# Performance work log

Hardware: AMD Instinct MI355X
Metric: run time of the kernel (lower is better)

The kernel has to match this reference:

```python
import jax, jax.numpy as jnp
import numpy as np

EMBED_DIM = 512
N_HEADS = 16
HEAD_DIM = EMBED_DIM // N_HEADS  # 32


def setup_inputs() -> dict:
    key0 = jax.random.key(0)
    ks = jax.random.split(key0, 8)
    B, S, D = 4, 2048, EMBED_DIM
    inp = {
        "key": jax.random.normal(ks[0], (B, S, D), dtype=jnp.float32),
        "query": jax.random.normal(ks[1], (B, S, D), dtype=jnp.float32),
        "value": jax.random.normal(ks[2], (B, S, D), dtype=jnp.float32),
        # per-head projection weights (nn.Linear: y = x @ W.T), no bias
        "Wq": jax.random.normal(ks[3], (HEAD_DIM, HEAD_DIM), dtype=jnp.float32) * 0.1,
        "Wk": jax.random.normal(ks[4], (HEAD_DIM, HEAD_DIM), dtype=jnp.float32) * 0.1,
        "Wv": jax.random.normal(ks[5], (HEAD_DIM, HEAD_DIM), dtype=jnp.float32) * 0.1,
        # output projection with bias
        "Wo": jax.random.normal(ks[6], (EMBED_DIM, EMBED_DIM), dtype=jnp.float32) * 0.05,
        "bo": jax.random.normal(ks[7], (EMBED_DIM,), dtype=jnp.float32) * 0.01,
    }
    return inp


def reference(key, query, value, Wq, Wk, Wv, Wo, bo):
    B, S, D = key.shape
    Sq = query.shape[1]
    H, dh = N_HEADS, HEAD_DIM
    # reshape to [B, S, H, dh] then per-head linear (x @ W.T)
    k = jnp.einsum('bshd,ed->bhse', key.reshape(B, S, H, dh), Wk)
    q = jnp.einsum('bshd,ed->bhse', query.reshape(B, Sq, H, dh), Wq)
    v = jnp.einsum('bshd,ed->bhse', value.reshape(B, S, H, dh), Wv)
    # naive attention: full [B,H,Sq,S] scores
    scores = jnp.einsum('bhqd,bhkd->bhqk', q, k) / jnp.sqrt(jnp.float32(dh))
    attn = jax.nn.softmax(scores, axis=-1)
    ctx = jnp.einsum('bhqk,bhkd->bhqd', attn, v)  # [B,H,Sq,dh]
    concat = ctx.transpose(0, 2, 1, 3).reshape(B, Sq, H * dh)
    return concat @ Wo.T + bo
```

## Files before the change

### kernel.cpp

```cpp
#include <hip/hip_runtime.h>
#include <hip/hip_bf16.h>


typedef __attribute__((ext_vector_type(8))) short bf16x8;
typedef __attribute__((ext_vector_type(4))) float f32x4;

#define MFMA16(a, b, c) __builtin_amdgcn_mfma_f32_16x16x32_bf16(a, b, c, 0, 0, 0)

static __device__ __forceinline__ unsigned short f2bf(float f) {
  __bf16 h = (__bf16)f;
  union { __bf16 h; unsigned short u; } c; c.h = h; return c.u;
}
static __device__ __forceinline__ float bf2f(unsigned short u) {
  union { unsigned u; float f; } c; c.u = ((unsigned)u) << 16; return c.f;
}

static __device__ __forceinline__ void gld_lds16(const ushort* g, ushort* l) {
  __builtin_amdgcn_global_load_lds(
      (const __attribute__((address_space(1))) unsigned int*)g,
      (__attribute__((address_space(3))) unsigned int*)l, 16, 0, 0);
}

static __device__ __forceinline__ void load8_split(const float* p, bf16x8& hi, bf16x8& lo) {
  float4 a = *(const float4*)p;
  float4 b = *(const float4*)(p + 4);
  float v[8] = {a.x, a.y, a.z, a.w, b.x, b.y, b.z, b.w};
  #pragma unroll
  for (int j = 0; j < 8; ++j) {
    unsigned short h = f2bf(v[j]);
    hi[j] = (short)h;
    lo[j] = (short)f2bf(v[j] - bf2f(h));
  }
}

__global__ __launch_bounds__(256) void proj_kernel(
    const float* __restrict__ key, const float* __restrict__ query,
    const float* __restrict__ value,
    const float* __restrict__ Wq, const float* __restrict__ Wk,
    const float* __restrict__ Wv, const float* __restrict__ Wo,
    ushort* __restrict__ Qp, ushort* __restrict__ Kp, ushort* __restrict__ Vt,
    ushort* __restrict__ Wob) {
  if (blockIdx.x >= 2048) {
    int i = ((blockIdx.x - 2048) * 256 + threadIdx.x) * 4;
    float4 v = *(const float4*)&Wo[i];
    ushort4 o;
    o.x = f2bf(v.x); o.y = f2bf(v.y); o.z = f2bf(v.z); o.w = f2bf(v.w);
    *(ushort4*)&Wob[i] = o;
    return;
  }
  __shared__ ushort tlds[4][16][40];
  const int tid = threadIdx.x;
  const int l = tid & 63, wid = tid >> 6;
  const int lr = l & 15, lc = l >> 4;
  const int task = blockIdx.x * 4 + wid;
  const int h = task & 15;
  const int st = (task >> 4) & 127;
  const int b = task >> 11;
  const int bh = b * 16 + h;
  const size_t xoff = ((size_t)b * 2048 + st * 16 + lr) * 512 + h * 32 + lc * 8;
  const float ALPHA = 0.2550354039f;

  #pragma unroll
  for (int t = 0; t < 3; ++t) {
    const float* x = (t == 0) ? query : (t == 1) ? key : value;
    const float* W = (t == 0) ? Wq : (t == 1) ? Wk : Wv;
    bf16x8 xh, xl;
    load8_split(x + xoff, xh, xl);
    f32x4 accs[2];
    #pragma unroll
    for (int eh = 0; eh < 2; ++eh) {
      bf16x8 wh, wl;
      load8_split(W + (size_t)(eh * 16 + lr) * 32 + lc * 8, wh, wl);
      f32x4 acc = {0.f, 0.f, 0.f, 0.f};
      acc = MFMA16(xh, wh, acc);
      acc = MFMA16(xh, wl, acc);
      acc = MFMA16(xl, wh, acc);
      accs[eh] = acc;
    }
    if (t == 2) {
      #pragma unroll
      for (int eh = 0; eh < 2; ++eh) {
        ushort4 pk;
        pk.x = f2bf(accs[eh][0]); pk.y = f2bf(accs[eh][1]);
        pk.z = f2bf(accs[eh][2]); pk.w = f2bf(accs[eh][3]);
        *(ushort4*)&Vt[((size_t)bh * 32 + eh * 16 + lr) * 2048 + st * 16 + lc * 4] = pk;
      }
    } else {
      const float scale = (t == 0) ? ALPHA : 1.0f;
      #pragma unroll
      for (int eh = 0; eh < 2; ++eh)
        #pragma unroll
        for (int r = 0; r < 4; ++r)
          tlds[wid][lc * 4 + r][eh * 16 + lr] = f2bf(accs[eh][r] * scale);
      bf16x8 row = *(const bf16x8*)&tlds[wid][l >> 2][(l & 3) * 8];
      ushort* dst = ((t == 0) ? Qp : Kp) +
                    ((size_t)bh * 2048 + st * 16 + (l >> 2)) * 32 + (l & 3) * 8;
      *(bf16x8*)dst = row;
    }
  }
}

__global__ __launch_bounds__(256) void attn_kernel(
    const ushort* __restrict__ Qp, const ushort* __restrict__ Kp,
    const ushort* __restrict__ Vt, ushort* __restrict__ Cb) {
  __shared__ ushort kbuf[3][2048];
  __shared__ ushort vbuf[3][2048];
  const int tid = threadIdx.x;
  const int l = tid & 63;
  const int lr = l & 15, lc = l >> 4;
  const int xcd = blockIdx.x & 7, idx = blockIdx.x >> 3;
  const int bh = xcd * 8 + (idx >> 4);
  const int qblk = idx & 15;
  const int b = bh >> 4, h = bh & 15;
  const int q0 = qblk * 128 + (tid >> 6) * 32;

  const ushort* Qb = Qp + (size_t)bh * 2048 * 32;
  const ushort* Kb = Kp + (size_t)bh * 2048 * 32;
  const ushort* Vb = Vt + (size_t)bh * 32 * 2048;

  const int s = tid ^ ((tid >> 3) & 7);
  const int m = s >> 2, pp = s & 3;
  const int g = (m & 32) | ((m & 12) << 1) | ((m & 16) >> 2) | (m & 3);
  const ushort* kg_src = Kb + (size_t)(g * 4 + pp) * 8;
  const ushort* vg_src = Vb + (size_t)(tid >> 3) * 2048 +
                         (((tid & 7) ^ ((tid >> 3) & 7)) * 8);

  int koff[4];
  #pragma unroll
  for (int kg = 0; kg < 4; ++kg) {
    int v = (kg * 16 + lr) * 4 + lc;
    v ^= (v >> 3) & 7;
    koff[kg] = v * 8;
  }
  int voff[2][2];
  #pragma unroll
  for (int kc = 0; kc < 2; ++kc)
    #pragma unroll
    for (int eh = 0; eh < 2; ++eh) {
      int v = (eh * 16 + lr) * 8 + kc * 4 + lc;
      v ^= (v >> 3) & 7;
      voff[kc][eh] = v * 8;
    }

  bf16x8 qf[2];
  qf[0] = *(const bf16x8*)&Qb[(size_t)(q0 + lr) * 32 + lc * 8];
  qf[1] = *(const bf16x8*)&Qb[(size_t)(q0 + 16 + lr) * 32 + lc * 8];

  bf16x8 ones;
  #pragma unroll
  for (int j = 0; j < 8; ++j) ones[j] = (short)0x3F80;

  f32x4 octx[2][2] = {};
  f32x4 dacc[2] = {};
  const f32x4 zero = {0.f, 0.f, 0.f, 0.f};

  gld_lds16(kg_src, &kbuf[0][tid * 8]);
  gld_lds16(vg_src, &vbuf[0][tid * 8]);
  gld_lds16(kg_src + (size_t)64 * 32, &kbuf[1][tid * 8]);
  gld_lds16(vg_src + 64, &vbuf[1][tid * 8]);
  asm volatile("s_waitcnt vmcnt(2)" ::: "memory");
  __builtin_amdgcn_s_barrier();

  int cur = 0, nx2 = 2;
  for (int kt = 0; kt < 32; ++kt) {
    if (kt < 30) {
      const int k0n = (kt + 2) * 64;
      gld_lds16(kg_src + (size_t)k0n * 32, &kbuf[nx2][tid * 8]);
      gld_lds16(vg_src + k0n, &vbuf[nx2][tid * 8]);
    }

    const ushort* kb = kbuf[cur];
    const ushort* vb = vbuf[cur];
    bf16x8 kf[4];
    #pragma unroll
    for (int kg = 0; kg < 4; ++kg)
      kf[kg] = *(const bf16x8*)&kb[koff[kg]];
    bf16x8 vf[2][2];
    #pragma unroll
    for (int kc = 0; kc < 2; ++kc)
      #pragma unroll
      for (int eh = 0; eh < 2; ++eh)
        vf[kc][eh] = *(const bf16x8*)&vb[voff[kc][eh]];

    #pragma unroll
    for (int qi = 0; qi < 2; ++qi) {
      f32x4 sc[4];
      #pragma unroll
      for (int kg = 0; kg < 4; ++kg)
        sc[kg] = MFMA16(kf[kg], qf[qi], zero);
      #pragma unroll
      for (int kc = 0; kc < 2; ++kc) {
        bf16x8 pa;
        #pragma unroll
        for (int r = 0; r < 4; ++r) {
          pa[r]     = (short)f2bf(__builtin_amdgcn_exp2f(sc[2 * kc][r]));
          pa[4 + r] = (short)f2bf(__builtin_amdgcn_exp2f(sc[2 * kc + 1][r]));
        }
        #pragma unroll
        for (int eh = 0; eh < 2; ++eh)
          octx[qi][eh] = MFMA16(pa, vf[kc][eh], octx[qi][eh]);
        dacc[qi] = MFMA16(pa, ones, dacc[qi]);
      }
    }

    if (kt < 30) {
      asm volatile("s_waitcnt vmcnt(2)" ::: "memory");
    } else {
      asm volatile("s_waitcnt vmcnt(0)" ::: "memory");
    }
    __builtin_amdgcn_s_barrier();
    cur = (cur == 2) ? 0 : cur + 1;
    nx2 = (nx2 == 2) ? 0 : nx2 + 1;
  }

  #pragma unroll
  for (int qi = 0; qi < 2; ++qi) {
    float inv[4];
    #pragma unroll
    for (int r = 0; r < 4; ++r)
      inv[r] = 1.0f / dacc[qi][r];
    #pragma unroll
    for (int eh = 0; eh < 2; ++eh)
      #pragma unroll
      for (int r = 0; r < 4; ++r) {
        float v = octx[qi][eh][r] * inv[r];
        Cb[((size_t)b * 2048 + q0 + qi * 16 + lc * 4 + r) * 512 + h * 32 + eh * 16 + lr] =
            f2bf(v);
      }
  }
}

__global__ __launch_bounds__(256) void oproj_kernel(
    const ushort* __restrict__ Cb, const ushort* __restrict__ Wob,
    const float* __restrict__ bo, float* __restrict__ out) {
  const int tid = threadIdx.x;
  const int l = tid & 63, w = tid >> 6;
  const int lr = l & 15, lc = l >> 4;
  const int qt = blockIdx.x >> 1;
  const int nt = blockIdx.x & 1;
  const int r0 = qt * 64;
  const int n0 = nt * 256 + w * 64;

  f32x4 acc[4][4] = {};
  for (int kk = 0; kk < 16; ++kk) {
    const int k0 = kk * 32;
    bf16x8 af[4], bf[4];
    #pragma unroll
    for (int i = 0; i < 4; ++i)
      af[i] = *(const bf16x8*)&Cb[(size_t)(r0 + i * 16 + lr) * 512 + k0 + lc * 8];
    #pragma unroll
    for (int j = 0; j < 4; ++j)
      bf[j] = *(const bf16x8*)&Wob[(size_t)(n0 + j * 16 + lr) * 512 + k0 + lc * 8];
    #pragma unroll
    for (int i = 0; i < 4; ++i)
      #pragma unroll
      for (int j = 0; j < 4; ++j)
        acc[i][j] = MFMA16(af[i], bf[j], acc[i][j]);
  }
  #pragma unroll
  for (int j = 0; j < 4; ++j) {
    float bias = bo[n0 + j * 16 + lr];
    #pragma unroll
    for (int i = 0; i < 4; ++i)
      #pragma unroll
      for (int r = 0; r < 4; ++r)
        out[(size_t)(r0 + i * 16 + lc * 4 + r) * 512 + n0 + j * 16 + lr] =
            acc[i][j][r] + bias;
  }
}

extern "C" void kernel_launch(void* const* d_in, const int* in_sizes, int n_in,
                              void* d_out, int out_size, void* d_ws, size_t ws_size,
                              hipStream_t stream) {
  (void)in_sizes; (void)n_in; (void)out_size; (void)ws_size;
  const float* key   = (const float*)d_in[0];
  const float* query = (const float*)d_in[1];
  const float* value = (const float*)d_in[2];
  const float* Wq    = (const float*)d_in[3];
  const float* Wk    = (const float*)d_in[4];
  const float* Wv    = (const float*)d_in[5];
  const float* Wo    = (const float*)d_in[6];
  const float* bo    = (const float*)d_in[7];
  float* out = (float*)d_out;

  const size_t NT = (size_t)4 * 16 * 2048 * 32;
  ushort* ws  = (ushort*)d_ws;
  ushort* Qp  = ws;
  ushort* Kp  = Qp + NT;
  ushort* Vt  = Kp + NT;
  ushort* Cb  = Vt + NT;
  ushort* Wob = Cb + NT;

  hipLaunchKernelGGL(proj_kernel, dim3(2304), dim3(256), 0, stream,
                     key, query, value, Wq, Wk, Wv, Wo, Qp, Kp, Vt, Wob);
  hipLaunchKernelGGL(attn_kernel, dim3(1024), dim3(256), 0, stream, Qp, Kp, Vt, Cb);
  hipLaunchKernelGGL(oproj_kernel, dim3(256), dim3(256), 0, stream, Cb, Wob, bo, out);
}
```

Measured before the change: 98.49 us.

## Use 512-thread attention blocks sharing each K/V tile across 256 queries

Doubles the attention block to 8 waves covering 256 queries, so each K/V tile staged in LDS is reused by twice as many query rows. Half the threads stage K and half stage V, giving one global-to-LDS load per thread per tile instead of two. The grid is halved to 512 blocks and the wait counts are adjusted. This halves the total K/V global traffic, at the cost of fewer blocks, larger barriers across 8 waves, and possibly lower occupancy.

```diff
diff --git a/kernel.cpp b/kernel.cpp
--- a/kernel.cpp
+++ b/kernel.cpp
@@ -100,30 +100,33 @@
   }
 }
 
-__global__ __launch_bounds__(256) void attn_kernel(
+__global__ __launch_bounds__(512) void attn_kernel(
     const ushort* __restrict__ Qp, const ushort* __restrict__ Kp,
     const ushort* __restrict__ Vt, ushort* __restrict__ Cb) {
-  __shared__ ushort kbuf[3][2048];
-  __shared__ ushort vbuf[3][2048];
+  __shared__ ushort kv[3][4096];
   const int tid = threadIdx.x;
-  const int l = tid & 63;
+  const int l = tid & 63, w = tid >> 6;
   const int lr = l & 15, lc = l >> 4;
   const int xcd = blockIdx.x & 7, idx = blockIdx.x >> 3;
-  const int bh = xcd * 8 + (idx >> 4);
-  const int qblk = idx & 15;
+  const int bh = xcd * 8 + (idx >> 3);
+  const int qblk = idx & 7;
   const int b = bh >> 4, h = bh & 15;
-  const int q0 = qblk * 128 + (tid >> 6) * 32;
+  const int q0 = qblk * 256 + w * 32;
 
   const ushort* Qb = Qp + (size_t)bh * 2048 * 32;
   const ushort* Kb = Kp + (size_t)bh * 2048 * 32;
   const ushort* Vb = Vt + (size_t)bh * 32 * 2048;
 
-  const int s = tid ^ ((tid >> 3) & 7);
-  const int m = s >> 2, pp = s & 3;
+  const bool stageK = tid < 256;
+  const int st = stageK ? tid : tid - 256;
+  const int si = st ^ ((st >> 3) & 7);
+  const int m = si >> 2, pp = si & 3;
   const int g = (m & 32) | ((m & 12) << 1) | ((m & 16) >> 2) | (m & 3);
-  const ushort* kg_src = Kb + (size_t)(g * 4 + pp) * 8;
-  const ushort* vg_src = Vb + (size_t)(tid >> 3) * 2048 +
-                         (((tid & 7) ^ ((tid >> 3) & 7)) * 8);
+  const ushort* src0 = stageK
+      ? Kb + (size_t)(g * 4 + pp) * 8
+      : Vb + (size_t)(st >> 3) * 2048 + (((st & 7) ^ ((st >> 3) & 7)) * 8);
+  const size_t sstep = stageK ? (size_t)64 * 32 : (size_t)64;
+  const int dofs = (stageK ? 0 : 2048) + st * 8;
 
   int koff[4];
   #pragma unroll
@@ -139,7 +142,7 @@
     for (int eh = 0; eh < 2; ++eh) {
       int v = (eh * 16 + lr) * 8 + kc * 4 + lc;
       v ^= (v >> 3) & 7;
-      voff[kc][eh] = v * 8;
+      voff[kc][eh] = 2048 + v * 8;
     }
 
   bf16x8 qf[2];
@@ -154,23 +157,17 @@
   f32x4 dacc[2] = {};
   const f32x4 zero = {0.f, 0.f, 0.f, 0.f};
 
-  gld_lds16(kg_src, &kbuf[0][tid * 8]);
-  gld_lds16(vg_src, &vbuf[0][tid * 8]);
-  gld_lds16(kg_src + (size_t)64 * 32, &kbuf[1][tid * 8]);
-  gld_lds16(vg_src + 64, &vbuf[1][tid * 8]);
-  asm volatile("s_waitcnt vmcnt(2)" ::: "memory");
+  gld_lds16(src0, &kv[0][dofs]);
+  gld_lds16(src0 + sstep, &kv[1][dofs]);
+  asm volatile("s_waitcnt vmcnt(1)" ::: "memory");
   __builtin_amdgcn_s_barrier();
 
   int cur = 0, nx2 = 2;
   for (int kt = 0; kt < 32; ++kt) {
-    if (kt < 30) {
-      const int k0n = (kt + 2) * 64;
-      gld_lds16(kg_src + (size_t)k0n * 32, &kbuf[nx2][tid * 8]);
-      gld_lds16(vg_src + k0n, &vbuf[nx2][tid * 8]);
-    }
-
-    const ushort* kb = kbuf[cur];
-    const ushort* vb = vbuf[cur];
+    if (kt < 30)
+      gld_lds16(src0 + (size_t)(kt + 2) * sstep, &kv[nx2][dofs]);
+
+    const ushort* kb = kv[cur];
     bf16x8 kf[4];
     #pragma unroll
     for (int kg = 0; kg < 4; ++kg)
@@ -180,7 +177,7 @@
     for (int kc = 0; kc < 2; ++kc)
       #pragma unroll
       for (int eh = 0; eh < 2; ++eh)
-        vf[kc][eh] = *(const bf16x8*)&vb[voff[kc][eh]];
+        vf[kc][eh] = *(const bf16x8*)&kb[voff[kc][eh]];
 
     #pragma unroll
     for (int qi = 0; qi < 2; ++qi) {
@@ -204,7 +201,7 @@
     }
 
     if (kt < 30) {
-      asm volatile("s_waitcnt vmcnt(2)" ::: "memory");
+      asm volatile("s_waitcnt vmcnt(1)" ::: "memory");
     } else {
       asm volatile("s_waitcnt vmcnt(0)" ::: "memory");
     }
@@ -293,6 +290,6 @@
 
   hipLaunchKernelGGL(proj_kernel, dim3(2304), dim3(256), 0, stream,
                      key, query, value, Wq, Wk, Wv, Wo, Qp, Kp, Vt, Wob);
-  hipLaunchKernelGGL(attn_kernel, dim3(1024), dim3(256), 0, stream, Qp, Kp, Vt, Cb);
+  hipLaunchKernelGGL(attn_kernel, dim3(512), dim3(512), 0, stream, Qp, Kp, Vt, Cb);
   hipLaunchKernelGGL(oproj_kernel, dim3(256), dim3(256), 0, stream, Cb, Wob, bo, out);
 }
```

After: 89.81 us, median of 2. 8.8% less time.
